# Performance work log

Measured on AMD Instinct MI355X. Metric: run time of the kernel, lower is better.

Reference implementation:

```python
import jax, jax.numpy as jnp
import numpy as np

MASK_2D_DIAMETER = 0.9


def _trilinear_sample(vol, pts):
    """torch.nn.functional.grid_sample 3D, mode='bilinear', align_corners=True,
    padding_mode='zeros'. vol: [L,L,L] laid out as [D,H,W]; pts: [...,3] with
    last dim ordered (x_grid, y_grid, z_grid) in [-1,1] -> (W,H,D) axes."""
    L = vol.shape[0]
    g = (pts + 1.0) * 0.5 * (L - 1)          # align_corners=True mapping
    g0 = jnp.floor(g)
    f = g - g0                                # fractional part, [...,3]
    g0 = g0.astype(jnp.int32)
    out = jnp.zeros(pts.shape[:-1], dtype=vol.dtype)
    for dx in (0, 1):
        for dy in (0, 1):
            for dz in (0, 1):
                ix = g0[..., 0] + dx
                iy = g0[..., 1] + dy
                iz = g0[..., 2] + dz
                w = ((f[..., 0] if dx else 1.0 - f[..., 0])
                     * (f[..., 1] if dy else 1.0 - f[..., 1])
                     * (f[..., 2] if dz else 1.0 - f[..., 2]))
                valid = (ix >= 0) & (ix < L) & (iy >= 0) & (iy < L) & (iz >= 0) & (iz < L)
                v = vol[jnp.clip(iz, 0, L - 1), jnp.clip(iy, 0, L - 1), jnp.clip(ix, 0, L - 1)]
                out = out + w * jnp.where(valid, v, jnp.zeros_like(v))
    return out


def _mask_2d(L):
    ax = jnp.linspace(-L / 2.0, L / 2.0, L)
    ax = ax - ax[L // 2]
    xx, yy = jnp.meshgrid(ax, ax, indexing='ij')
    return (jnp.sqrt(xx ** 2 + yy ** 2) < (L / 2.0) * MASK_2D_DIAMETER).astype(jnp.float32)


def setup_inputs() -> dict:
    key = jax.random.key(0)
    k1, k2 = jax.random.split(key)
    B, L = 2048, 128
    rotmat = jax.random.normal(k1, (B, 3, 3), dtype=jnp.float32)
    vol = jax.random.normal(k2, (L, L, L), dtype=jnp.float32)
    return {"rotmat": rotmat, "vol": vol}


def reference(rotmat, vol):
    L = vol.shape[0]
    B = rotmat.shape[0]
    lin = jnp.linspace(-1.0, 1.0, L)
    # original coords[i,j,k] = (y,x,z) = (lin[j], lin[i], lin[k]); only the
    # slice i = L//2 of the [B,L,L,L] rotated volume survives, so we only
    # build that plane: grid point = (x_grid=lin[j], y_grid=lin[L//2], z_grid=lin[k]).
    jj, kk = jnp.meshgrid(lin, lin, indexing='ij')        # [L,L]
    plane = jnp.stack([jj, jnp.full_like(jj, lin[L // 2]), kk], axis=-1).reshape(-1, 3)  # [L*L,3]
    # pytorch3d Rotate.transform_points: row vectors, p @ R
    rot_pts = jnp.einsum('nc,bcd->bnd', plane, rotmat)    # [B, L*L, 3]
    proj = _trilinear_sample(vol, rot_pts).reshape(B, 1, L, L)
    proj = proj * _mask_2d(L)
    return proj
```

## Files before the change

kernel.cpp:

```cpp
#include <hip/hip_runtime.h>

constexpr int L = 128;
constexpr int NVOX = L * L * L;
constexpr size_t TAB_BYTES = (size_t)NVOX * 16;
constexpr int SORT_N = 2048;
constexpr int RANK_BLOCKS = SORT_N / 256;
constexpr int TAB_BLOCKS = NVOX / 256;

union HU { unsigned short u; _Float16 h; };
typedef _Float16 h2v __attribute__((ext_vector_type(2)));
union H2U { unsigned int u; h2v h; };

__device__ __forceinline__ unsigned int pack2(float a, float b) {
    HU x, y; x.h = (_Float16)a; y.h = (_Float16)b;
    return (unsigned int)x.u | ((unsigned int)y.u << 16);
}
__device__ __forceinline__ h2v u2h2(unsigned int w) { H2U c; c.u = w; return c.h; }

__device__ __forceinline__ int brick_idx(int x, int y, int z) {
    return (z << 14) | ((y >> 1) << 8) | ((x >> 1) << 2) | ((y & 1) << 1) | (x & 1);
}

__device__ __forceinline__ unsigned part5(unsigned x) {
    x &= 0x1F;
    x = (x | (x << 4)) & 0x0F0Fu;
    x = (x | (x << 2)) & 0x3333u;
    x = (x | (x << 1)) & 0x5555u;
    return x;
}

__device__ __forceinline__ unsigned make_key(const float* __restrict__ R, int i)
{
    float nx = R[1] * R[8] - R[2] * R[7];
    float ny = R[2] * R[6] - R[0] * R[8];
    float nz = R[0] * R[7] - R[1] * R[6];
    if (nz < 0.0f) { nx = -nx; ny = -ny; nz = -nz; }
    const float s = fabsf(nx) + fabsf(ny) + nz + 1e-30f;
    const float u = nx / s, v = ny / s;
    const int qu = min(max((int)((u * 0.5f + 0.5f) * 32.0f), 0), 31);
    const int qv = min(max((int)((v * 0.5f + 0.5f) * 32.0f), 0), 31);
    const unsigned morton = (part5((unsigned)qv) << 1) | part5((unsigned)qu);
    return (morton << 11) | (unsigned)i;
}

__global__ __launch_bounds__(256) void build_tab_sort(
    const float* __restrict__ vol, uint4* __restrict__ T,
    const float* __restrict__ rotmat, int* __restrict__ perm, int B, int do_sort)
{
    const int bid = blockIdx.x;
    const int tid = threadIdx.x;

    if (bid < RANK_BLOCKS) {
        if (!do_sort) return;
        __shared__ unsigned keys[SORT_N];
        #pragma unroll
        for (int h = 0; h < SORT_N / 256; ++h) {
            const int i = tid + h * 256;
            keys[i] = (i < B) ? make_key(rotmat + i * 9, i) : 0xFFFFFFFFu;
        }
        __syncthreads();
        const int img = (bid << 8) + tid;
        if (img < B) {
            const unsigned mykey = keys[img];
            int rank = 0;
            for (int j = 0; j < SORT_N; ++j)
                rank += (keys[j] < mykey) ? 1 : 0;
            perm[rank] = img;
        }
        return;
    }

    const int e = (bid - RANK_BLOCKS) * 256 + tid;
    const int x  = e & 127, y = (e >> 7) & 127, z = e >> 14;
    const int x1 = min(x + 1, 127);
    const int ro0 = (y << 7), ro1 = (min(y + 1, 127) << 7);
    const float* __restrict__ p0 = vol + (z << 14);
    const float* __restrict__ p1 = vol + (min(z + 1, 127) << 14);
    uint4 o;
    o.x = pack2(p0[ro0 | x], p0[ro0 | x1]);
    o.y = pack2(p0[ro1 | x], p0[ro1 | x1]);
    o.z = pack2(p1[ro0 | x], p1[ro0 | x1]);
    o.w = pack2(p1[ro1 | x], p1[ro1 | x1]);
    T[brick_idx(x, y, z)] = o;
}

struct Px {
    int e;
    h2v wab;
    float ya, yb, za, zb;
};

__device__ __forceinline__ Px setup_slow(float gx, float gy, float gz, bool vis)
{
    Px p;
    const float fx0 = floorf(gx), fy0 = floorf(gy), fz0 = floorf(gz);
    const int ix = (int)fx0, iy = (int)fy0, iz = (int)fz0;
    const float fx = gx - fx0, fy = gy - fy0, fz = gz - fz0;

    const float wx0 = ((unsigned)ix       < 128u) ? 1.0f - fx : 0.0f;
    const float wx1 = ((unsigned)(ix + 1) < 128u) ? fx        : 0.0f;
    const float wy0 = ((unsigned)iy       < 128u) ? 1.0f - fy : 0.0f;
    const float wy1 = ((unsigned)(iy + 1) < 128u) ? fy        : 0.0f;
    const float wz0 = ((unsigned)iz       < 128u) ? 1.0f - fz : 0.0f;
    const float wz1 = ((unsigned)(iz + 1) < 128u) ? fz        : 0.0f;

    const float xa = (ix == -1) ? wx1 : wx0;
    const float xb = (ix == -1) ? 0.0f : wx1;
    p.wab = h2v{(_Float16)xa, (_Float16)xb};
    p.ya = (iy == -1) ? wy1 : wy0;  p.yb = (iy == -1) ? 0.0f : wy1;
    p.za = (iz == -1) ? wz1 : wz0;  p.zb = (iz == -1) ? 0.0f : wz1;
    if (!vis) { p.za = 0.0f; p.zb = 0.0f; }

    const bool alive = vis && (ix >= -1) && (ix <= 127) && (iy >= -1)
                           && (iy <= 127) && (iz >= -1) && (iz <= 127);
    const int xe = min(max(ix, 0), 127);
    const int ye = min(max(iy, 0), 127);
    const int ze = min(max(iz, 0), 127);
    p.e = alive ? brick_idx(xe, ye, ze) : 0;
    return p;
}

__device__ __forceinline__ Px setup_fast(float gx, float gy, float gz)
{
    Px p;
    const float fx0 = floorf(gx), fy0 = floorf(gy), fz0 = floorf(gz);
    const float fx = gx - fx0, fy = gy - fy0, fz = gz - fz0;
    p.wab = h2v{(_Float16)(1.0f - fx), (_Float16)fx};
    p.ya = 1.0f - fy;  p.yb = fy;
    p.za = 1.0f - fz;  p.zb = fz;
    p.e = brick_idx((int)fx0, (int)fy0, (int)fz0);
    return p;
}

__device__ __forceinline__ float combine_px(const Px& p, uint4 W)
{
    const float d0 = __builtin_amdgcn_fdot2(u2h2(W.x), p.wab, 0.0f, false);
    const float d1 = __builtin_amdgcn_fdot2(u2h2(W.y), p.wab, 0.0f, false);
    const float d2 = __builtin_amdgcn_fdot2(u2h2(W.z), p.wab, 0.0f, false);
    const float d3 = __builtin_amdgcn_fdot2(u2h2(W.w), p.wab, 0.0f, false);
    return p.za * (p.ya * d0 + p.yb * d1) + p.zb * (p.ya * d2 + p.yb * d3);
}

__global__ __launch_bounds__(256) void xfel_proj_t(
    const float* __restrict__ rotmat,
    const uint4* __restrict__ T,
    float* __restrict__ out,
    const int* __restrict__ perm,
    int nimg_per_xcd)
{
    const int n = blockIdx.x;
    int b, t;
    if (nimg_per_xcd > 0) {
        const int xcd = n & 7;
        const int s   = n >> 3;
        b = perm[xcd * nimg_per_xcd + (s >> 4)];
        t = s & 15;
    } else {
        b = n >> 4;
        t = n & 15;
    }

    const int tid  = threadIdx.x;
    const int lane = tid & 63;
    const int wv   = tid >> 6;
    const int k    = ((t & 1) << 6) | lane;
    const int j0   = ((t >> 1) << 4) + (wv << 2);

    const int obase = (b * L + j0) * L + k;

    const float stepw = 128.0f / 127.0f;
    const float ak  = (float)(k - 64) * stepw;
    const float ak2 = ak * ak;
    const float thr = 57.6f * 57.6f;

    bool vis[4];
    bool all_vis = true, any_vis = false;
    #pragma unroll
    for (int m = 0; m < 4; ++m) {
        const float aj = (float)(j0 + m - 64) * stepw;
        vis[m] = (aj * aj + ak2 < thr);
        any_vis |= vis[m];
        all_vis &= vis[m];
    }
    if (__ballot((int)any_vis) == 0ull) {
        #pragma unroll
        for (int m = 0; m < 4; ++m)
            __builtin_nontemporal_store(0.0f, out + obase + m * L);
        return;
    }

    const float* __restrict__ R = rotmat + b * 9;
    const float R00 = R[0], R01 = R[1], R02 = R[2];
    const float R10 = R[3], R11 = R[4], R12 = R[5];
    const float R20 = R[6], R21 = R[7], R22 = R[8];

    const float lk  = -1.0f + (float)k * (2.0f / 127.0f);
    const float yc  = -1.0f + 64.0f * (2.0f / 127.0f);
    const float lj0 = -1.0f + (float)j0 * (2.0f / 127.0f);

    float gx = (lj0 * R00 + yc * R10 + lk * R20 + 1.0f) * 63.5f;
    float gy = (lj0 * R01 + yc * R11 + lk * R21 + 1.0f) * 63.5f;
    float gz = (lj0 * R02 + yc * R12 + lk * R22 + 1.0f) * 63.5f;

    const float gx3 = gx + 3.0f * R00, gy3 = gy + 3.0f * R01, gz3 = gz + 3.0f * R02;
    const bool intr = all_vis
        && (gx  >= 0.0f) && (gx  < 127.0f) && (gx3 >= 0.0f) && (gx3 < 127.0f)
        && (gy  >= 0.0f) && (gy  < 127.0f) && (gy3 >= 0.0f) && (gy3 < 127.0f)
        && (gz  >= 0.0f) && (gz  < 127.0f) && (gz3 >= 0.0f) && (gz3 < 127.0f);

    Px p[4];
    if (__ballot((int)intr) == ~0ull) {
        #pragma unroll
        for (int m = 0; m < 4; ++m) {
            p[m] = setup_fast(gx, gy, gz);
            gx += R00; gy += R01; gz += R02;
        }
    } else {
        bool any_alive = false;
        #pragma unroll
        for (int m = 0; m < 4; ++m) {
            p[m] = setup_slow(gx, gy, gz, vis[m]);
            any_alive |= (p[m].e != 0);
            gx += R00; gy += R01; gz += R02;
        }
        if (__ballot((int)any_alive) == 0ull) {
            #pragma unroll
            for (int m = 0; m < 4; ++m)
                __builtin_nontemporal_store(0.0f, out + obase + m * L);
            return;
        }
    }

    uint4 W[4];
    #pragma unroll
    for (int m = 0; m < 4; ++m) W[m] = T[p[m].e];

    __builtin_amdgcn_sched_barrier(0);

    #pragma unroll
    for (int m = 0; m < 4; ++m) {
        const float res = combine_px(p[m], W[m]);
        __builtin_nontemporal_store(res, out + obase + m * L);
    }
}

typedef float f2v __attribute__((ext_vector_type(2), aligned(4)));

struct PxF {
    int b00, b01, b10, b11, xe;
    float wa, wb, wy0, wy1, wz0, wz1;
    bool alive;
};

__device__ __forceinline__ PxF setup_pxf(float gx, float gy, float gz, bool vis)
{
    PxF p;
    const float fx0 = floorf(gx), fy0 = floorf(gy), fz0 = floorf(gz);
    const int ix = (int)fx0, iy = (int)fy0, iz = (int)fz0;
    const float fx = gx - fx0, fy = gy - fy0, fz = gz - fz0;
    const float wx0 = ((unsigned)ix       < 128u) ? 1.0f - fx : 0.0f;
    const float wx1 = ((unsigned)(ix + 1) < 128u) ? fx        : 0.0f;
    p.wa = (ix == -1) ? wx1 : ((ix == 127) ? 0.0f : wx0);
    p.wb = (ix == 127) ? wx0 : ((ix == -1) ? 0.0f : wx1);
    p.wy0 = ((unsigned)iy       < 128u) ? 1.0f - fy : 0.0f;
    p.wy1 = ((unsigned)(iy + 1) < 128u) ? fy        : 0.0f;
    p.wz0 = (vis && (unsigned)iz       < 128u) ? 1.0f - fz : 0.0f;
    p.wz1 = (vis && (unsigned)(iz + 1) < 128u) ? fz        : 0.0f;
    p.alive = vis && (ix >= -1) && (ix <= 127) && (iy >= -1) && (iy <= 127)
                  && (iz >= -1) && (iz <= 127);
    int xe = min(max(ix, 0), 126);
    int y0 = min(max(iy, 0), 127), y1 = min(max(iy + 1, 0), 127);
    int z0 = min(max(iz, 0), 127), z1 = min(max(iz + 1, 0), 127);
    if (!p.alive) { xe = 0; y0 = 0; y1 = 0; z0 = 0; z1 = 0; }
    p.xe  = xe;
    p.b00 = (z0 << 14) | (y0 << 7);
    p.b01 = (z0 << 14) | (y1 << 7);
    p.b10 = (z1 << 14) | (y0 << 7);
    p.b11 = (z1 << 14) | (y1 << 7);
    return p;
}

__global__ __launch_bounds__(256) void xfel_proj_f(
    const float* __restrict__ rotmat,
    const float* __restrict__ vol,
    float* __restrict__ out)
{
    const int tid  = threadIdx.x;
    const int lane = tid & 63;
    const int wv   = tid >> 6;
    const int t    = blockIdx.x;
    const int b    = blockIdx.y;
    const int k    = ((t & 1) << 6) | lane;
    const int j0   = ((t >> 1) << 4) + (wv << 2);
    const int obase = (b * L + j0) * L + k;

    const float stepw = 128.0f / 127.0f;
    const float ak  = (float)(k - 64) * stepw;
    const float ak2 = ak * ak;
    const float thr = 57.6f * 57.6f;

    bool vis[4]; bool any_vis = false;
    #pragma unroll
    for (int m = 0; m < 4; ++m) {
        const float aj = (float)(j0 + m - 64) * stepw;
        vis[m] = (aj * aj + ak2 < thr);
        any_vis |= vis[m];
    }
    if (__ballot((int)any_vis) == 0ull) {
        #pragma unroll
        for (int m = 0; m < 4; ++m)
            __builtin_nontemporal_store(0.0f, out + obase + m * L);
        return;
    }

    const float* __restrict__ R = rotmat + b * 9;
    const float R00 = R[0], R01 = R[1], R02 = R[2];
    const float R10 = R[3], R11 = R[4], R12 = R[5];
    const float R20 = R[6], R21 = R[7], R22 = R[8];
    const float lk  = -1.0f + (float)k * (2.0f / 127.0f);
    const float yc  = -1.0f + 64.0f * (2.0f / 127.0f);
    const float lj0 = -1.0f + (float)j0 * (2.0f / 127.0f);

    float gx = (lj0 * R00 + yc * R10 + lk * R20 + 1.0f) * 63.5f;
    float gy = (lj0 * R01 + yc * R11 + lk * R21 + 1.0f) * 63.5f;
    float gz = (lj0 * R02 + yc * R12 + lk * R22 + 1.0f) * 63.5f;

    PxF p[4]; bool any_alive = false;
    #pragma unroll
    for (int m = 0; m < 4; ++m) {
        p[m] = setup_pxf(gx, gy, gz, vis[m]);
        any_alive |= p[m].alive;
        gx += R00; gy += R01; gz += R02;
    }
    if (__ballot((int)any_alive) == 0ull) {
        #pragma unroll
        for (int m = 0; m < 4; ++m)
            __builtin_nontemporal_store(0.0f, out + obase + m * L);
        return;
    }

    f2v v[4][4];
    #pragma unroll
    for (int m = 0; m < 4; ++m) {
        v[m][0] = *(const f2v*)(vol + p[m].b00 + p[m].xe);
        v[m][1] = *(const f2v*)(vol + p[m].b01 + p[m].xe);
        v[m][2] = *(const f2v*)(vol + p[m].b10 + p[m].xe);
        v[m][3] = *(const f2v*)(vol + p[m].b11 + p[m].xe);
    }
    __builtin_amdgcn_sched_barrier(0);

    #pragma unroll
    for (int m = 0; m < 4; ++m) {
        const float r00 = p[m].wa * v[m][0].x + p[m].wb * v[m][0].y;
        const float r01 = p[m].wa * v[m][1].x + p[m].wb * v[m][1].y;
        const float r10 = p[m].wa * v[m][2].x + p[m].wb * v[m][2].y;
        const float r11 = p[m].wa * v[m][3].x + p[m].wb * v[m][3].y;
        const float res = p[m].wz0 * (p[m].wy0 * r00 + p[m].wy1 * r01)
                        + p[m].wz1 * (p[m].wy0 * r10 + p[m].wy1 * r11);
        __builtin_nontemporal_store(res, out + obase + m * L);
    }
}

extern "C" void kernel_launch(void* const* d_in, const int* in_sizes, int n_in,
                              void* d_out, int out_size, void* d_ws, size_t ws_size,
                              hipStream_t stream) {
    const float* rotmat = (const float*)d_in[0];
    const float* vol    = (const float*)d_in[1];
    float* out          = (float*)d_out;
    const int B = in_sizes[0] / 9;

    const size_t need = TAB_BYTES + (size_t)SORT_N * 4;
    if (ws_size >= TAB_BYTES) {
        uint4* T  = (uint4*)d_ws;
        int* perm = (int*)((char*)d_ws + TAB_BYTES);
        const bool can_sort = (ws_size >= need) && (B % 8 == 0) && (B <= SORT_N);
        build_tab_sort<<<dim3(RANK_BLOCKS + TAB_BLOCKS), dim3(256), 0, stream>>>(
            vol, T, rotmat, perm, B, can_sort ? 1 : 0);
        const int nper = can_sort ? (B / 8) : 0;
        xfel_proj_t<<<dim3(16 * B), dim3(256), 0, stream>>>(rotmat, T, out,
                                                            perm, nper);
    } else {
        xfel_proj_f<<<dim3(16, B), dim3(256), 0, stream>>>(rotmat, vol, out);
    }
}
```

Baseline: 103.2 us.

## Halve gather table to 8-byte per-voxel z-slabs in 2x2x2 bricks

Replaces the 16-byte per-voxel table, which held the full 2x2x2 fp16 neighbourhood, with an 8-byte entry holding only the 2x2 xy neighbourhood. Entries are arranged in 2x2x2 bricks, and each sample does two 8-byte gathers, one at z and one at z+1. The table is half the size, so it is cheaper to build and has a smaller cache footprint for the random gathers. In exchange the projection kernel issues twice as many gather instructions, and the z-edge handling now relies on clamping the index plus the zero weights.

```diff
diff --git a/kernel.cpp b/kernel.cpp
--- a/kernel.cpp
+++ b/kernel.cpp
@@ -2,10 +2,10 @@
 
 constexpr int L = 128;
 constexpr int NVOX = L * L * L;
-constexpr size_t TAB_BYTES = (size_t)NVOX * 16;
+constexpr size_t TAB_BYTES = (size_t)NVOX * 8;
 constexpr int SORT_N = 2048;
 constexpr int RANK_BLOCKS = SORT_N / 256;
-constexpr int TAB_BLOCKS = NVOX / 256;
+constexpr int TAB_BLOCKS = (NVOX / 2) / 256;
 
 union HU { unsigned short u; _Float16 h; };
 typedef _Float16 h2v __attribute__((ext_vector_type(2)));
@@ -17,8 +17,9 @@
 }
 __device__ __forceinline__ h2v u2h2(unsigned int w) { H2U c; c.u = w; return c.h; }
 
-__device__ __forceinline__ int brick_idx(int x, int y, int z) {
-    return (z << 14) | ((y >> 1) << 8) | ((x >> 1) << 2) | ((y & 1) << 1) | (x & 1);
+__device__ __forceinline__ int brick8(int x, int y, int z) {
+    return ((z >> 1) << 15) | ((y >> 1) << 9) | ((x >> 1) << 3)
+         | ((z & 1) << 2) | ((y & 1) << 1) | (x & 1);
 }
 
 __device__ __forceinline__ unsigned part5(unsigned x) {
@@ -44,7 +45,7 @@
 }
 
 __global__ __launch_bounds__(256) void build_tab_sort(
-    const float* __restrict__ vol, uint4* __restrict__ T,
+    const float* __restrict__ vol, uint2* __restrict__ T,
     const float* __restrict__ rotmat, int* __restrict__ perm, int B, int do_sort)
 {
     const int bid = blockIdx.x;
@@ -71,21 +72,23 @@
     }
 
     const int e = (bid - RANK_BLOCKS) * 256 + tid;
-    const int x  = e & 127, y = (e >> 7) & 127, z = e >> 14;
+    const int x  = e & 127, y = (e >> 7) & 127, zp = e >> 14;
+    const int z0 = zp << 1, z1 = z0 | 1;
     const int x1 = min(x + 1, 127);
     const int ro0 = (y << 7), ro1 = (min(y + 1, 127) << 7);
-    const float* __restrict__ p0 = vol + (z << 14);
-    const float* __restrict__ p1 = vol + (min(z + 1, 127) << 14);
-    uint4 o;
-    o.x = pack2(p0[ro0 | x], p0[ro0 | x1]);
-    o.y = pack2(p0[ro1 | x], p0[ro1 | x1]);
-    o.z = pack2(p1[ro0 | x], p1[ro0 | x1]);
-    o.w = pack2(p1[ro1 | x], p1[ro1 | x1]);
-    T[brick_idx(x, y, z)] = o;
+    const float* __restrict__ p0 = vol + (z0 << 14);
+    const float* __restrict__ p1 = vol + (z1 << 14);
+    uint2 a, b;
+    a.x = pack2(p0[ro0 | x], p0[ro0 | x1]);
+    a.y = pack2(p0[ro1 | x], p0[ro1 | x1]);
+    b.x = pack2(p1[ro0 | x], p1[ro0 | x1]);
+    b.y = pack2(p1[ro1 | x], p1[ro1 | x1]);
+    T[brick8(x, y, z0)] = a;
+    T[brick8(x, y, z1)] = b;
 }
 
 struct Px {
-    int e;
+    int e0, e1;
     h2v wab;
     float ya, yb, za, zb;
 };
@@ -108,15 +111,17 @@
     const float xb = (ix == -1) ? 0.0f : wx1;
     p.wab = h2v{(_Float16)xa, (_Float16)xb};
     p.ya = (iy == -1) ? wy1 : wy0;  p.yb = (iy == -1) ? 0.0f : wy1;
-    p.za = (iz == -1) ? wz1 : wz0;  p.zb = (iz == -1) ? 0.0f : wz1;
+    p.za = wz0;  p.zb = wz1;
     if (!vis) { p.za = 0.0f; p.zb = 0.0f; }
 
     const bool alive = vis && (ix >= -1) && (ix <= 127) && (iy >= -1)
                            && (iy <= 127) && (iz >= -1) && (iz <= 127);
-    const int xe = min(max(ix, 0), 127);
-    const int ye = min(max(iy, 0), 127);
-    const int ze = min(max(iz, 0), 127);
-    p.e = alive ? brick_idx(xe, ye, ze) : 0;
+    const int xe  = min(max(ix, 0), 127);
+    const int ye  = min(max(iy, 0), 127);
+    const int ze0 = min(max(iz, 0), 127);
+    const int ze1 = min(max(iz + 1, 0), 127);
+    p.e0 = alive ? brick8(xe, ye, ze0) : 0;
+    p.e1 = alive ? brick8(xe, ye, ze1) : 0;
     return p;
 }
 
@@ -125,25 +130,27 @@
     Px p;
     const float fx0 = floorf(gx), fy0 = floorf(gy), fz0 = floorf(gz);
     const float fx = gx - fx0, fy = gy - fy0, fz = gz - fz0;
+    const int ix = (int)fx0, iy = (int)fy0, iz = (int)fz0;
     p.wab = h2v{(_Float16)(1.0f - fx), (_Float16)fx};
     p.ya = 1.0f - fy;  p.yb = fy;
     p.za = 1.0f - fz;  p.zb = fz;
-    p.e = brick_idx((int)fx0, (int)fy0, (int)fz0);
+    p.e0 = brick8(ix, iy, iz);
+    p.e1 = brick8(ix, iy, iz + 1);
     return p;
 }
 
-__device__ __forceinline__ float combine_px(const Px& p, uint4 W)
-{
-    const float d0 = __builtin_amdgcn_fdot2(u2h2(W.x), p.wab, 0.0f, false);
-    const float d1 = __builtin_amdgcn_fdot2(u2h2(W.y), p.wab, 0.0f, false);
-    const float d2 = __builtin_amdgcn_fdot2(u2h2(W.z), p.wab, 0.0f, false);
-    const float d3 = __builtin_amdgcn_fdot2(u2h2(W.w), p.wab, 0.0f, false);
-    return p.za * (p.ya * d0 + p.yb * d1) + p.zb * (p.ya * d2 + p.yb * d3);
+__device__ __forceinline__ float combine_px(const Px& p, uint2 W0, uint2 W1)
+{
+    const float r0 = p.ya * __builtin_amdgcn_fdot2(u2h2(W0.x), p.wab, 0.0f, false)
+                   + p.yb * __builtin_amdgcn_fdot2(u2h2(W0.y), p.wab, 0.0f, false);
+    const float r1 = p.ya * __builtin_amdgcn_fdot2(u2h2(W1.x), p.wab, 0.0f, false)
+                   + p.yb * __builtin_amdgcn_fdot2(u2h2(W1.y), p.wab, 0.0f, false);
+    return p.za * r0 + p.zb * r1;
 }
 
 __global__ __launch_bounds__(256) void xfel_proj_t(
     const float* __restrict__ rotmat,
-    const uint4* __restrict__ T,
+    const uint2* __restrict__ T,
     float* __restrict__ out,
     const int* __restrict__ perm,
     int nimg_per_xcd)
@@ -220,7 +227,7 @@
         #pragma unroll
         for (int m = 0; m < 4; ++m) {
             p[m] = setup_slow(gx, gy, gz, vis[m]);
-            any_alive |= (p[m].e != 0);
+            any_alive |= (p[m].e0 != 0);
             gx += R00; gy += R01; gz += R02;
         }
         if (__ballot((int)any_alive) == 0ull) {
@@ -231,15 +238,15 @@
         }
     }
 
-    uint4 W[4];
-    #pragma unroll
-    for (int m = 0; m < 4; ++m) W[m] = T[p[m].e];
+    uint2 W0[4], W1[4];
+    #pragma unroll
+    for (int m = 0; m < 4; ++m) { W0[m] = T[p[m].e0]; W1[m] = T[p[m].e1]; }
 
     __builtin_amdgcn_sched_barrier(0);
 
     #pragma unroll
     for (int m = 0; m < 4; ++m) {
-        const float res = combine_px(p[m], W[m]);
+        const float res = combine_px(p[m], W0[m], W1[m]);
         __builtin_nontemporal_store(res, out + obase + m * L);
     }
 }
@@ -371,7 +378,7 @@
 
     const size_t need = TAB_BYTES + (size_t)SORT_N * 4;
     if (ws_size >= TAB_BYTES) {
-        uint4* T  = (uint4*)d_ws;
+        uint2* T  = (uint2*)d_ws;
         int* perm = (int*)((char*)d_ws + TAB_BYTES);
         const bool can_sort = (ws_size >= need) && (B % 8 == 0) && (B <= SORT_N);
         build_tab_sort<<<dim3(RANK_BLOCKS + TAB_BLOCKS), dim3(256), 0, stream>>>(
```

Measured after the change: 105.2 us. About the same (+1.9%).
